# Optimization experiments

Measured on AMD Instinct MI355X. Metric: run time of the kernel, lower is better.

The kernel has to match this reference:

```python
import jax, jax.numpy as jnp
import numpy as np

N = 50000          # nodes
E_RAND = 800000    # random edges (self-loops appended -> total 850000)
F_IN = 256         # features_num
H = 128            # hidden
HEADS = 4          # headslayers
C = 40             # num_class
OUTDIM = H + HEADS * H + H  # 768, cat of [x_lin, conv1, conv2]
LRELU = 0.01       # F.leaky_relu default slope
ATT_SLOPE = 0.2    # PyG GATConv negative_slope
BN_EPS = 1e-5


def setup_inputs() -> dict:
    key = jax.random.key(0)
    ks = jax.random.split(key, 20)
    src = jax.random.randint(ks[0], (E_RAND,), 0, N)
    dst = jax.random.randint(ks[1], (E_RAND,), 0, N)
    loops = jnp.arange(N, dtype=src.dtype)
    edge_index = jnp.stack([jnp.concatenate([src, loops]),
                            jnp.concatenate([dst, loops])], axis=0)
    g = lambda k, shape, fan: jax.random.normal(k, shape, jnp.float32) * (1.0 / np.sqrt(fan))
    return {
        "x": jax.random.normal(ks[2], (N, F_IN), jnp.float32),
        "edge_index": edge_index,
        # first_lin
        "fw_W": g(ks[3], (F_IN, H), F_IN), "fw_b": jnp.zeros((H,), jnp.float32),
        # conv1: GATConv(H, H, heads=HEADS)
        "c1_W": g(ks[4], (H, HEADS * H), H),
        "c1_as": g(ks[5], (HEADS, H), H), "c1_ad": g(ks[6], (HEADS, H), H),
        "c1_b": jnp.zeros((HEADS * H,), jnp.float32),
        # conv2: GATConv(HEADS*H, H, heads=1)
        "c2_W": g(ks[7], (HEADS * H, H), HEADS * H),
        "c2_as": g(ks[8], (1, H), H), "c2_ad": g(ks[9], (1, H), H),
        "c2_b": jnp.zeros((H,), jnp.float32),
        # batchnorms (training-mode batch stats)
        "bn1_g": jnp.ones((H,), jnp.float32), "bn1_b": jnp.zeros((H,), jnp.float32),
        "bn2_g": jnp.ones((HEADS * H,), jnp.float32), "bn2_b": jnp.zeros((HEADS * H,), jnp.float32),
        "bn3_g": jnp.ones((H,), jnp.float32), "bn3_b": jnp.zeros((H,), jnp.float32),
        # lin2
        "l2_W": g(ks[10], (OUTDIM, C), OUTDIM), "l2_b": jnp.zeros((C,), jnp.float32),
    }


def _batchnorm(x, gamma, beta):
    mu = jnp.mean(x, axis=0)
    var = jnp.mean(jnp.square(x - mu), axis=0)  # biased, as torch BN training
    return (x - mu) * (gamma / jnp.sqrt(var + BN_EPS)) + beta


def _gat_conv(x, edge_index, W, a_src, a_dst, bias, heads, out_dim):
    src, dst = edge_index[0], edge_index[1]
    h = (x @ W).reshape(-1, heads, out_dim)            # [N, heads, out]
    alpha_s = jnp.sum(h * a_src, axis=-1)              # [N, heads]
    alpha_d = jnp.sum(h * a_dst, axis=-1)              # [N, heads]
    e = alpha_s[src] + alpha_d[dst]                    # [E, heads]
    e = jnp.where(e >= 0, e, ATT_SLOPE * e)            # leaky_relu(0.2)
    # segment softmax over incoming edges of each dst node
    emax = jax.ops.segment_max(e, dst, num_segments=N)
    e = jnp.exp(e - emax[dst])
    denom = jax.ops.segment_sum(e, dst, num_segments=N)
    alpha = e / (denom[dst] + 1e-16)                   # [E, heads]
    msg = h[src] * alpha[:, :, None]                   # [E, heads, out]
    out = jax.ops.segment_sum(msg, dst, num_segments=N)
    return out.reshape(-1, heads * out_dim) + bias


def _lrelu(x):
    return jnp.where(x >= 0, x, LRELU * x)


def reference(x, edge_index, fw_W, fw_b, c1_W, c1_as, c1_ad, c1_b,
              c2_W, c2_as, c2_ad, c2_b, bn1_g, bn1_b, bn2_g, bn2_b,
              bn3_g, bn3_b, l2_W, l2_b):
    h = _lrelu(x @ fw_W + fw_b)
    h = _batchnorm(h, bn1_g, bn1_b)
    feats = [h]
    h = _lrelu(_gat_conv(h, edge_index, c1_W, c1_as, c1_ad, c1_b, HEADS, H))
    h = _batchnorm(h, bn2_g, bn2_b)
    feats.append(h)
    h = _lrelu(_gat_conv(h, edge_index, c2_W, c2_as, c2_ad, c2_b, 1, H))
    h = _batchnorm(h, bn3_g, bn3_b)
    feats.append(h)
    z = jnp.concatenate(feats, axis=1) @ l2_W + l2_b
    return jax.nn.log_softmax(z, axis=-1)
```

## Files before the change

### kernel.cpp

```cpp
#include <hip/hip_runtime.h>

#define INF_F __builtin_inff()

typedef unsigned short u16;
typedef __attribute__((ext_vector_type(8))) short s16x8;
typedef __attribute__((ext_vector_type(4))) float f32x4;

union U8 { uint4 q; s16x8 v; };

__device__ __forceinline__ float b2f(u16 u) {
    union { unsigned int i; float f; } v; v.i = ((unsigned int)u) << 16; return v.f;
}
__device__ __forceinline__ u16 f2b(float f) {
    union { float f; unsigned int i; } v; v.f = f;
    unsigned int r = (v.i + 0x7FFFu + ((v.i >> 16) & 1u)) >> 16;
    return (u16)r;
}
__device__ __forceinline__ void bf2x(unsigned int p, float& lo, float& hi) {
    union { unsigned int i; float f; } a, b;
    a.i = p << 16; b.i = p & 0xFFFF0000u;
    lo = a.f; hi = b.f;
}
__device__ __forceinline__ unsigned int packbf(float lo, float hi) {
    return (unsigned int)f2b(lo) | ((unsigned int)f2b(hi) << 16);
}

__device__ __forceinline__ void pack_one(const float* __restrict__ W, int K, int N,
                                         int Npad, u16* __restrict__ pb, int idx)
{
    int k = idx / Npad, n = idx - k * Npad;
    float v = (n < N) ? W[(size_t)k * N + n] : 0.f;
    int K5 = K >> 5;
    size_t o = ((size_t)(n >> 4) * K5 + (k >> 5)) * 512
             + ((size_t)((k >> 3) & 3)) * 128 + (n & 15) * 8 + (k & 7);
    pb[o] = f2b(v);
}

__launch_bounds__(256)
__global__ void k_prep(const float* __restrict__ fw_W, const float* __restrict__ c1_W,
                       const float* __restrict__ c2_W, const float* __restrict__ l2_W,
                       u16* __restrict__ pb_l1, u16* __restrict__ pb_c1,
                       u16* __restrict__ pb_c2, u16* __restrict__ pb_f,
                       const int* __restrict__ dst, int E, int* __restrict__ counts)
{
    int idx = blockIdx.x * 256 + threadIdx.x;
    if (idx < 32768) { pack_one(fw_W, 256, 128, 128, pb_l1, idx); return; }
    idx -= 32768;
    if (idx < 65536) { pack_one(c1_W, 128, 512, 512, pb_c1, idx); return; }
    idx -= 65536;
    if (idx < 65536) { pack_one(c2_W, 512, 128, 128, pb_c2, idx); return; }
    idx -= 65536;
    if (idx < 49152) { pack_one(l2_W, 768, 40, 64, pb_f, idx); return; }
    idx -= 49152;
    if (idx < E) atomicAdd(&counts[dst[idx]], 1);
}

template<int NFRAG, bool A_FP32, bool BN_A, bool BIAS, bool LRELU, int HEADS_PB>
__launch_bounds__(256)
__global__ void k_mgemm(const void* __restrict__ Av, int lda, int K,
                        const u16* __restrict__ pb,
                        u16* __restrict__ C, int ldc, int M,
                        const float* __restrict__ scale, const float* __restrict__ shift,
                        const float* __restrict__ bias,
                        const float* __restrict__ aw_s, const float* __restrict__ aw_d,
                        float* __restrict__ as_o, float* __restrict__ ad_o, int nheads)
{
    const int tid = threadIdx.x;
    const int w = tid >> 6, l = tid & 63;
    const int lo = l & 15, hi = l >> 4;
    const int row0 = blockIdx.y * 128 + w * 32;
    if (row0 >= M) return;
    const int cb0 = blockIdx.x * NFRAG;
    const int K5 = K >> 5;

    f32x4 acc[NFRAG][2];
    #pragma unroll
    for (int i = 0; i < NFRAG; ++i)
        #pragma unroll
        for (int s = 0; s < 2; ++s) acc[i][s] = (f32x4){0.f, 0.f, 0.f, 0.f};

    int arow[2];
    #pragma unroll
    for (int s = 0; s < 2; ++s) {
        int r = row0 + s * 16 + lo;
        arow[s] = r < M ? r : M - 1;
    }

    for (int k5 = 0; k5 < K5; ++k5) {
        const int ak = k5 * 32 + hi * 8;
        s16x8 af[2];
        #pragma unroll
        for (int s = 0; s < 2; ++s) {
            float x[8];
            if (A_FP32) {
                const float* A = (const float*)Av + (size_t)arow[s] * lda + ak;
                float4 v0 = *reinterpret_cast<const float4*>(A);
                float4 v1 = *reinterpret_cast<const float4*>(A + 4);
                x[0]=v0.x; x[1]=v0.y; x[2]=v0.z; x[3]=v0.w;
                x[4]=v1.x; x[5]=v1.y; x[6]=v1.z; x[7]=v1.w;
            } else {
                uint4 q = *reinterpret_cast<const uint4*>((const u16*)Av + (size_t)arow[s] * lda + ak);
                bf2x(q.x, x[0], x[1]); bf2x(q.y, x[2], x[3]);
                bf2x(q.z, x[4], x[5]); bf2x(q.w, x[6], x[7]);
            }
            if (BN_A) {
                #pragma unroll
                for (int j = 0; j < 8; ++j) x[j] = fmaf(x[j], scale[ak + j], shift[ak + j]);
            }
            U8 au;
            au.q.x = packbf(x[0], x[1]); au.q.y = packbf(x[2], x[3]);
            au.q.z = packbf(x[4], x[5]); au.q.w = packbf(x[6], x[7]);
            af[s] = au.v;
        }
        #pragma unroll
        for (int cb = 0; cb < NFRAG; ++cb) {
            s16x8 bf = *reinterpret_cast<const s16x8*>(
                pb + ((size_t)(cb0 + cb) * K5 + k5) * 512 + l * 8);
            acc[cb][0] = __builtin_amdgcn_mfma_f32_16x16x32_bf16(af[0], bf, acc[cb][0], 0, 0, 0);
            acc[cb][1] = __builtin_amdgcn_mfma_f32_16x16x32_bf16(af[1], bf, acc[cb][1], 0, 0, 0);
        }
    }

    #pragma unroll
    for (int cb = 0; cb < NFRAG; ++cb) {
        int col = (cb0 + cb) * 16 + lo;
        #pragma unroll
        for (int s = 0; s < 2; ++s) {
            #pragma unroll
            for (int p = 0; p < 4; ++p) {
                int r = row0 + s * 16 + hi * 4 + p;
                if (r < M) {
                    float v = acc[cb][s][p];
                    if (BIAS)  v += bias[col];
                    if (LRELU) v = v >= 0.f ? v : 0.01f * v;
                    C[(size_t)r * ldc + col] = f2b(v);
                }
            }
        }
    }

    if (HEADS_PB > 0) {
        const int h = (cb0 >> 3);
        #pragma unroll
        for (int s = 0; s < 2; ++s) {
            float ps[4] = {0.f,0.f,0.f,0.f}, pd[4] = {0.f,0.f,0.f,0.f};
            #pragma unroll
            for (int cb = 0; cb < NFRAG; ++cb) {
                int col = (cb0 + cb) * 16 + lo;
                float ws = aw_s[col], wd = aw_d[col];
                #pragma unroll
                for (int p = 0; p < 4; ++p) {
                    ps[p] = fmaf(acc[cb][s][p], ws, ps[p]);
                    pd[p] = fmaf(acc[cb][s][p], wd, pd[p]);
                }
            }
            #pragma unroll
            for (int m = 1; m < 16; m <<= 1) {
                #pragma unroll
                for (int p = 0; p < 4; ++p) {
                    ps[p] += __shfl_xor(ps[p], m, 64);
                    pd[p] += __shfl_xor(pd[p], m, 64);
                }
            }
            if (lo == 0) {
                #pragma unroll
                for (int p = 0; p < 4; ++p) {
                    int r = row0 + s * 16 + hi * 4 + p;
                    if (r < M) {
                        as_o[(size_t)r * nheads + h] = ps[p];
                        ad_o[(size_t)r * nheads + h] = pd[p];
                    }
                }
            }
        }
    }
}

__launch_bounds__(256)
__global__ void k_mfinal(const u16* __restrict__ h1, const u16* __restrict__ h2,
                         const u16* __restrict__ h3,
                         const float* __restrict__ scale, const float* __restrict__ shift,
                         const u16* __restrict__ pb, const float* __restrict__ bias,
                         float* __restrict__ out, int M)
{
    const int tid = threadIdx.x;
    const int w = tid >> 6, l = tid & 63;
    const int lo = l & 15, hi = l >> 4;
    const int row0 = blockIdx.x * 128 + w * 32;
    if (row0 >= M) return;
    const int K5 = 24;

    f32x4 acc[4][2];
    #pragma unroll
    for (int i = 0; i < 4; ++i)
        #pragma unroll
        for (int s = 0; s < 2; ++s) acc[i][s] = (f32x4){0.f, 0.f, 0.f, 0.f};

    int arow[2];
    #pragma unroll
    for (int s = 0; s < 2; ++s) {
        int r = row0 + s * 16 + lo;
        arow[s] = r < M ? r : M - 1;
    }

    for (int k5 = 0; k5 < K5; ++k5) {
        const int kk = k5 * 32 + hi * 8;
        const u16* src; int ld, offk;
        if (kk < 128)      { src = h1; ld = 128; offk = kk; }
        else if (kk < 640) { src = h2; ld = 512; offk = kk - 128; }
        else               { src = h3; ld = 128; offk = kk - 640; }
        s16x8 af[2];
        #pragma unroll
        for (int s = 0; s < 2; ++s) {
            uint4 q = *reinterpret_cast<const uint4*>(src + (size_t)arow[s] * ld + offk);
            float x[8];
            bf2x(q.x, x[0], x[1]); bf2x(q.y, x[2], x[3]);
            bf2x(q.z, x[4], x[5]); bf2x(q.w, x[6], x[7]);
            #pragma unroll
            for (int j = 0; j < 8; ++j) x[j] = fmaf(x[j], scale[kk + j], shift[kk + j]);
            U8 au;
            au.q.x = packbf(x[0], x[1]); au.q.y = packbf(x[2], x[3]);
            au.q.z = packbf(x[4], x[5]); au.q.w = packbf(x[6], x[7]);
            af[s] = au.v;
        }
        #pragma unroll
        for (int cb = 0; cb < 4; ++cb) {
            s16x8 bf = *reinterpret_cast<const s16x8*>(pb + ((size_t)cb * K5 + k5) * 512 + l * 8);
            acc[cb][0] = __builtin_amdgcn_mfma_f32_16x16x32_bf16(af[0], bf, acc[cb][0], 0, 0, 0);
            acc[cb][1] = __builtin_amdgcn_mfma_f32_16x16x32_bf16(af[1], bf, acc[cb][1], 0, 0, 0);
        }
    }

    #pragma unroll
    for (int s = 0; s < 2; ++s) {
        #pragma unroll
        for (int p = 0; p < 4; ++p) {
            int r = row0 + s * 16 + hi * 4 + p;
            float z0 = acc[0][s][p] + bias[lo];
            float z1 = acc[1][s][p] + bias[16 + lo];
            float z2 = -INF_F;
            if (lo < 8) z2 = acc[2][s][p] + bias[32 + lo];
            float mx = fmaxf(fmaxf(z0, z1), z2);
            #pragma unroll
            for (int m = 1; m < 16; m <<= 1) mx = fmaxf(mx, __shfl_xor(mx, m, 64));
            float se = __expf(z0 - mx) + __expf(z1 - mx) + ((lo < 8) ? __expf(z2 - mx) : 0.f);
            #pragma unroll
            for (int m = 1; m < 16; m <<= 1) se += __shfl_xor(se, m, 64);
            float lse = mx + __logf(se);
            if (r < M) {
                out[(size_t)r * 40 + lo]      = z0 - lse;
                out[(size_t)r * 40 + 16 + lo] = z1 - lse;
                if (lo < 8) out[(size_t)r * 40 + 32 + lo] = z2 - lse;
            }
        }
    }
}

__launch_bounds__(256)
__global__ void k_colstats(const u16* __restrict__ X, int M, int C,
                           float* __restrict__ psum, float* __restrict__ psq)
{
    const int CG  = C >> 3;
    const int RPI = 256 / CG;
    const int tid = threadIdx.x;
    const int cg  = tid & (CG - 1);
    const int ro  = tid / CG;
    const int nb  = gridDim.x;
    const int rows_chunk = (M + nb - 1) / nb;
    const int r0 = blockIdx.x * rows_chunk;
    const int r1 = min(M, r0 + rows_chunk);

    float s[8] = {}, q[8] = {};
    for (int r = r0 + ro; r < r1; r += RPI) {
        uint4 u = *reinterpret_cast<const uint4*>(X + (size_t)r * C + cg * 8);
        float x[8];
        bf2x(u.x, x[0], x[1]); bf2x(u.y, x[2], x[3]);
        bf2x(u.z, x[4], x[5]); bf2x(u.w, x[6], x[7]);
        #pragma unroll
        for (int j = 0; j < 8; ++j) { s[j] += x[j]; q[j] = fmaf(x[j], x[j], q[j]); }
    }

    __shared__ float lsum[8][256];
    __shared__ float lsq [8][256];
    #pragma unroll
    for (int j = 0; j < 8; ++j) { lsum[j][tid] = s[j]; lsq[j][tid] = q[j]; }
    __syncthreads();

    if (tid < CG) {
        #pragma unroll
        for (int j = 0; j < 8; ++j) {
            float ss = 0.f, qq = 0.f;
            for (int o = 0; o < RPI; ++o) {
                ss += lsum[j][o * CG + tid];
                qq += lsq [j][o * CG + tid];
            }
            psum[(size_t)blockIdx.x * C + tid * 8 + j] = ss;
            psq [(size_t)blockIdx.x * C + tid * 8 + j] = qq;
        }
    }
}

__launch_bounds__(256)
__global__ void k_colred(const float* __restrict__ psum, const float* __restrict__ psq,
                         const float* __restrict__ g, const float* __restrict__ b,
                         int nb, int M, int C,
                         float* __restrict__ scale, float* __restrict__ shift)
{
    int c = blockIdx.x * 4 + (threadIdx.x >> 6);
    int lane = threadIdx.x & 63;
    if (c >= C) return;
    float s = 0.f, q = 0.f;
    for (int l = lane; l < nb; l += 64) {
        s += psum[(size_t)l * C + c];
        q += psq [(size_t)l * C + c];
    }
    #pragma unroll
    for (int off = 32; off; off >>= 1) {
        s += __shfl_xor(s, off, 64);
        q += __shfl_xor(q, off, 64);
    }
    if (lane == 0) {
        float mu  = s / (float)M;
        float var = q / (float)M - mu * mu;
        float sc  = g[c] * rsqrtf(var + 1e-5f);
        scale[c] = sc;
        shift[c] = b[c] - mu * sc;
    }
}

__launch_bounds__(256)
__global__ void k_scan1(const int* __restrict__ counts, int n,
                        int* __restrict__ rowstart, int* __restrict__ tilesum)
{
    const int tid = threadIdx.x;
    const int lane = tid & 63, w = tid >> 6;
    const int i0 = blockIdx.x * 1024 + tid * 4;
    int v0 = 0, v1 = 0, v2 = 0, v3 = 0;
    if (i0 + 3 < n) {
        int4 q = *reinterpret_cast<const int4*>(counts + i0);
        v0 = q.x; v1 = q.y; v2 = q.z; v3 = q.w;
    } else if (i0 < n) {
        v0 = counts[i0];
        if (i0 + 1 < n) v1 = counts[i0 + 1];
        if (i0 + 2 < n) v2 = counts[i0 + 2];
    }
    int s1 = v0 + v1, s2 = s1 + v2, s3 = s2 + v3;
    int x = s3;
    #pragma unroll
    for (int off = 1; off < 64; off <<= 1) {
        int t = __shfl_up(x, off, 64);
        if (lane >= off) x += t;
    }
    __shared__ int wsum[4];
    if (lane == 63) wsum[w] = x;
    __syncthreads();
    int woff = 0;
    #pragma unroll
    for (int i = 0; i < 4; ++i)
        if (i < w) woff += wsum[i];
    int excl = woff + x - s3;
    if (i0 + 0 < n) rowstart[i0 + 1] = excl + v0;
    if (i0 + 1 < n) rowstart[i0 + 2] = excl + s1;
    if (i0 + 2 < n) rowstart[i0 + 3] = excl + s2;
    if (i0 + 3 < n) rowstart[i0 + 4] = excl + s3;
    if (tid == 255) tilesum[blockIdx.x] = wsum[0] + wsum[1] + wsum[2] + wsum[3];
}

__launch_bounds__(256)
__global__ void k_scan3(int* __restrict__ rowstart, const int* __restrict__ tilesum, int n)
{
    const int tile = (int)((blockIdx.x * 256) >> 10);
    __shared__ int s_off;
    if (threadIdx.x < 64) {
        int lane = threadIdx.x;
        int v = (lane < tile) ? tilesum[lane] : 0;
        #pragma unroll
        for (int m = 1; m < 64; m <<= 1) v += __shfl_xor(v, m, 64);
        if (lane == 0) s_off = v;
    }
    __syncthreads();
    int i = blockIdx.x * 256 + threadIdx.x;
    if (i < n) rowstart[i + 1] += s_off;
    if (blockIdx.x == 0 && threadIdx.x == 0) rowstart[0] = 0;
}

__launch_bounds__(256)
__global__ void k_scatter(const int* __restrict__ ei, int E,
                          const int* __restrict__ rowstart,
                          int* __restrict__ fill, int* __restrict__ csr)
{
    int e = blockIdx.x * 256 + threadIdx.x;
    if (e >= E) return;
    int s = ei[e], d = ei[E + e];
    int pos = rowstart[d] + atomicAdd(&fill[d], 1);
    csr[pos] = s;
}

__launch_bounds__(256)
__global__ void k_gat_agg_h4(const u16* __restrict__ hp,
                             const float* __restrict__ as_, const float* __restrict__ ad_,
                             const int* __restrict__ rowstart, const int* __restrict__ csr,
                             const float* __restrict__ bias, u16* __restrict__ out, int Nn)
{
    int d = (int)((blockIdx.x * (size_t)blockDim.x + threadIdx.x) >> 6);
    int lane = threadIdx.x & 63;
    if (d >= Nn) return;
    const int h = lane >> 4;
    const int li = lane & 15;
    const int dim = li * 8;
    int e0 = rowstart[d], e1 = rowstart[d + 1];
    float adv = ad_[(size_t)d * 4 + h];

    float mx = -INF_F;
    for (int j = e0 + li; j < e1; j += 16) {
        int s = csr[j];
        float e = as_[(size_t)s * 4 + h] + adv;
        e = e >= 0.f ? e : 0.2f * e;
        mx = fmaxf(mx, e);
    }
    #pragma unroll
    for (int m = 1; m < 16; m <<= 1) mx = fmaxf(mx, __shfl_xor(mx, m, 64));

    float lsum = 0.f;
    float acc[8] = {};

    #define F4(J, A, U) { int jj = min((J), e1 - 1); int s_ = csr[jj];                \
        A = as_[(size_t)s_ * 4 + h];                                                  \
        U = *reinterpret_cast<const uint4*>(hp + ((size_t)s_ * 4 + h) * 128 + dim); }
    #define C4(A, U) { float e_ = A + adv; e_ = e_ >= 0.f ? e_ : 0.2f * e_;           \
        float w_ = __expf(e_ - mx); lsum += w_;                                       \
        float x_[8];                                                                  \
        bf2x(U.x, x_[0], x_[1]); bf2x(U.y, x_[2], x_[3]);                             \
        bf2x(U.z, x_[4], x_[5]); bf2x(U.w, x_[6], x_[7]);                             \
        _Pragma("unroll")                                                             \
        for (int t_ = 0; t_ < 8; ++t_) acc[t_] = fmaf(x_[t_], w_, acc[t_]); }

    float a0, a1, a2, a3, a4, a5, a6, a7;
    uint4 u0, u1, u2, u3, u4, u5, u6, u7;
    F4(e0 + 0, a0, u0); F4(e0 + 1, a1, u1); F4(e0 + 2, a2, u2); F4(e0 + 3, a3, u3);
    F4(e0 + 4, a4, u4); F4(e0 + 5, a5, u5); F4(e0 + 6, a6, u6); F4(e0 + 7, a7, u7);

    int j = e0;
    for (; j + 3 < e1; j += 4) {
        C4(a0, u0); C4(a1, u1); C4(a2, u2); C4(a3, u3);
        a0 = a4; u0 = u4; a1 = a5; u1 = u5; a2 = a6; u2 = u6; a3 = a7; u3 = u7;
        F4(j + 8, a4, u4); F4(j + 9, a5, u5); F4(j + 10, a6, u6); F4(j + 11, a7, u7);
    }
    if (j < e1)     C4(a0, u0);
    if (j + 1 < e1) C4(a1, u1);
    if (j + 2 < e1) C4(a2, u2);
    #undef F4
    #undef C4

    float inv = 1.f / (lsum + 1e-16f);
    const int ob = h * 128 + dim;
    float v[8];
    #pragma unroll
    for (int t = 0; t < 8; ++t) {
        float z = acc[t] * inv + bias[ob + t];
        v[t] = z >= 0.f ? z : 0.01f * z;
    }
    uint4 o;
    o.x = packbf(v[0], v[1]); o.y = packbf(v[2], v[3]);
    o.z = packbf(v[4], v[5]); o.w = packbf(v[6], v[7]);
    *reinterpret_cast<uint4*>(out + (size_t)d * 512 + ob) = o;
}

__launch_bounds__(256)
__global__ void k_gat_agg_h1(const u16* __restrict__ hp,
                             const float* __restrict__ as_, const float* __restrict__ ad_,
                             const int* __restrict__ rowstart, const int* __restrict__ csr,
                             const float* __restrict__ bias, u16* __restrict__ out, int Nn)
{
    int d = (int)((blockIdx.x * (size_t)blockDim.x + threadIdx.x) >> 6);
    int lane = threadIdx.x & 63;
    if (d >= Nn) return;
    const int dim = lane * 2;
    int e0 = rowstart[d], e1 = rowstart[d + 1];
    float adv = ad_[d];

    float mx = -INF_F;
    for (int j = e0 + lane; j < e1; j += 64) {
        int s = csr[j];
        float e = as_[s] + adv;
        e = e >= 0.f ? e : 0.2f * e;
        mx = fmaxf(mx, e);
    }
    #pragma unroll
    for (int m = 1; m < 64; m <<= 1) mx = fmaxf(mx, __shfl_xor(mx, m, 64));

    float lsum = 0.f, acc0 = 0.f, acc1 = 0.f;

    #define F1(J, A, U) { int jj = min((J), e1 - 1); int s_ = csr[jj];                \
        A = as_[s_];                                                                  \
        U = *reinterpret_cast<const unsigned int*>(hp + (size_t)s_ * 128 + dim); }
    #define C1(A, U) { float e_ = A + adv; e_ = e_ >= 0.f ? e_ : 0.2f * e_;           \
        float w_ = __expf(e_ - mx); float x0_, x1_; bf2x(U, x0_, x1_);                \
        lsum += w_; acc0 = fmaf(x0_, w_, acc0); acc1 = fmaf(x1_, w_, acc1); }

    float a0, a1, a2, a3, a4, a5, a6, a7;
    unsigned int u0, u1, u2, u3, u4, u5, u6, u7;
    F1(e0 + 0, a0, u0); F1(e0 + 1, a1, u1); F1(e0 + 2, a2, u2); F1(e0 + 3, a3, u3);
    F1(e0 + 4, a4, u4); F1(e0 + 5, a5, u5); F1(e0 + 6, a6, u6); F1(e0 + 7, a7, u7);

    int j = e0;
    for (; j + 3 < e1; j += 4) {
        C1(a0, u0); C1(a1, u1); C1(a2, u2); C1(a3, u3);
        a0 = a4; u0 = u4; a1 = a5; u1 = u5; a2 = a6; u2 = u6; a3 = a7; u3 = u7;
        F1(j + 8, a4, u4); F1(j + 9, a5, u5); F1(j + 10, a6, u6); F1(j + 11, a7, u7);
    }
    if (j < e1)     C1(a0, u0);
    if (j + 1 < e1) C1(a1, u1);
    if (j + 2 < e1) C1(a2, u2);
    #undef F1
    #undef C1

    float inv = 1.f / (lsum + 1e-16f);
    float v0 = acc0 * inv + bias[dim];
    float v1 = acc1 * inv + bias[dim + 1];
    v0 = v0 >= 0.f ? v0 : 0.01f * v0;
    v1 = v1 >= 0.f ? v1 : 0.01f * v1;
    *reinterpret_cast<unsigned int*>(out + (size_t)d * 128 + dim) = packbf(v0, v1);
}

extern "C" void kernel_launch(void* const* d_in, const int* in_sizes, int n_in,
                              void* d_out, int out_size, void* d_ws, size_t ws_size,
                              hipStream_t stream)
{
    const float* x     = (const float*)d_in[0];
    const int*   ei    = (const int*)  d_in[1];
    const float* fw_W  = (const float*)d_in[2];
    const float* fw_b  = (const float*)d_in[3];
    const float* c1_W  = (const float*)d_in[4];
    const float* c1_as = (const float*)d_in[5];
    const float* c1_ad = (const float*)d_in[6];
    const float* c1_b  = (const float*)d_in[7];
    const float* c2_W  = (const float*)d_in[8];
    const float* c2_as = (const float*)d_in[9];
    const float* c2_ad = (const float*)d_in[10];
    const float* c2_b  = (const float*)d_in[11];
    const float* bn1_g = (const float*)d_in[12];
    const float* bn1_b = (const float*)d_in[13];
    const float* bn2_g = (const float*)d_in[14];
    const float* bn2_b = (const float*)d_in[15];
    const float* bn3_g = (const float*)d_in[16];
    const float* bn3_b = (const float*)d_in[17];
    const float* l2_W  = (const float*)d_in[18];
    const float* l2_b  = (const float*)d_in[19];
    float* out = (float*)d_out;

    const int N = in_sizes[0] / 256;
    const int E = in_sizes[1] / 2;
    const int NB = 256;

    char* base = (char*)d_ws;
    size_t off = 0;
    auto alloc = [&](size_t bytes) -> void* {
        void* p = (void*)(base + off);
        off = (off + bytes + 255) & ~(size_t)255;
        return p;
    };
    int*   counts = (int*)  alloc((size_t)N * 4);
    int*   fill   = (int*)  alloc((size_t)N * 4);
    size_t zero_bytes = off;
    const int SCB = (N + 1023) / 1024;
    float* as1      = (float*)alloc((size_t)N * 4 * 4);
    float* ad1      = (float*)alloc((size_t)N * 4 * 4);
    float* as2      = (float*)alloc((size_t)N * 4);
    float* ad2      = (float*)alloc((size_t)N * 4);
    float* psum     = (float*)alloc((size_t)NB * 512 * 4);
    float* psq      = (float*)alloc((size_t)NB * 512 * 4);
    int*   rowstart = (int*)  alloc((size_t)(N + 1) * 4);
    int*   tilesum  = (int*)  alloc((size_t)SCB * 4);
    int*   csr      = (int*)  alloc((size_t)E * 4);
    float* scale768 = (float*)alloc(768 * 4);
    float* shift768 = (float*)alloc(768 * 4);
    u16*   pb_l1    = (u16*)  alloc((size_t)256 * 128 * 2);
    u16*   pb_c1    = (u16*)  alloc((size_t)128 * 512 * 2);
    u16*   pb_c2    = (u16*)  alloc((size_t)512 * 128 * 2);
    u16*   pb_f     = (u16*)  alloc((size_t)768 * 64 * 2);
    u16*   h1       = (u16*)  alloc((size_t)N * 128 * 2);
    u16*   h2       = (u16*)  alloc((size_t)N * 512 * 2);
    u16*   hp1      = (u16*)  alloc((size_t)N * 512 * 2);
    u16*   hp2      = hp1;
    u16*   h3       = hp1 + (size_t)N * 128;
    (void)ws_size; (void)n_in; (void)out_size;

    const int mb2 = (N + 127) / 128;
    const int wave_blocks = (int)(((size_t)N * 64 + 255) / 256);
    const int PK = 32768 + 65536 + 65536 + 49152;

    hipMemsetAsync(base, 0, zero_bytes, stream);

    k_prep<<<(PK + E + 255) / 256, 256, 0, stream>>>(
        fw_W, c1_W, c2_W, l2_W, pb_l1, pb_c1, pb_c2, pb_f, ei + E, E, counts);

    k_scan1<<<SCB, 256, 0, stream>>>(counts, N, rowstart, tilesum);
    k_scan3<<<(N + 255) / 256, 256, 0, stream>>>(rowstart, tilesum, N);

    k_scatter<<<(E + 255) / 256, 256, 0, stream>>>(ei, E, rowstart, fill, csr);

    k_mgemm<8, true, false, true, true, 0><<<dim3(1, mb2), 256, 0, stream>>>(
        x, 256, 256, pb_l1, h1, 128, N, nullptr, nullptr, fw_b,
        nullptr, nullptr, nullptr, nullptr, 0);

    k_colstats<<<NB, 256, 0, stream>>>(h1, N, 128, psum, psq);
    k_colred<<<(128 + 3) / 4, 256, 0, stream>>>(psum, psq, bn1_g, bn1_b, NB, N, 128,
                                                scale768, shift768);

    k_mgemm<8, false, true, false, false, 1><<<dim3(4, mb2), 256, 0, stream>>>(
        h1, 128, 128, pb_c1, hp1, 512, N, scale768, shift768, nullptr,
        c1_as, c1_ad, as1, ad1, 4);
    k_gat_agg_h4<<<wave_blocks, 256, 0, stream>>>(
        hp1, as1, ad1, rowstart, csr, c1_b, h2, N);

    k_colstats<<<NB, 256, 0, stream>>>(h2, N, 512, psum, psq);
    k_colred<<<(512 + 3) / 4, 256, 0, stream>>>(psum, psq, bn2_g, bn2_b, NB, N, 512,
                                                scale768 + 128, shift768 + 128);

    k_mgemm<8, false, true, false, false, 1><<<dim3(1, mb2), 256, 0, stream>>>(
        h2, 512, 512, pb_c2, hp2, 128, N, scale768 + 128, shift768 + 128, nullptr,
        c2_as, c2_ad, as2, ad2, 1);
    k_gat_agg_h1<<<wave_blocks, 256, 0, stream>>>(
        hp2, as2, ad2, rowstart, csr, c2_b, h3, N);

    k_colstats<<<NB, 256, 0, stream>>>(h3, N, 128, psum, psq);
    k_colred<<<(128 + 3) / 4, 256, 0, stream>>>(psum, psq, bn3_g, bn3_b, NB, N, 128,
                                                scale768 + 640, shift768 + 640);

    k_mfinal<<<mb2, 256, 0, stream>>>(h1, h2, h3, scale768, shift768, pb_f, l2_b, out, N);
}
```

Baseline: 453.6 us.

## Fuse CSR scatter into first GEMM launch and pack two nodes per wave in head-1 aggregation

The CSR scatter is merged into the first linear-layer GEMM as extra blocks of a single launch, so both run concurrently and one launch is removed. Zeroing of the fill counters moves from the memset into the scan kernel. The single-head GAT aggregation now handles two destination nodes per wave, 32 lanes each, with 4 features per lane and 8-byte loads, which halves wave count and widens the gathers. In exchange, the two half-waves loop to the longer of their two edge lists and mask the extra iterations.

```diff
diff --git a/kernel.cpp b/kernel.cpp
--- a/kernel.cpp
+++ b/kernel.cpp
@@ -55,13 +55,86 @@
     if (idx < E) atomicAdd(&counts[dst[idx]], 1);
 }
 
-template<int NFRAG, bool A_FP32, bool BN_A, bool BIAS, bool LRELU, int HEADS_PB>
-__launch_bounds__(256)
-__global__ void k_mgemm(const void* __restrict__ Av, int lda, int K,
+__launch_bounds__(256)
+__global__ void k_l1sc(const float* __restrict__ x, const u16* __restrict__ pb,
+                       u16* __restrict__ h1, int M, const float* __restrict__ bias,
+                       int mb2, const int* __restrict__ ei, int E,
+                       const int* __restrict__ rowstart, int* __restrict__ fill,
+                       int* __restrict__ csr)
+{
+    if ((int)blockIdx.x >= mb2) {
+        int e = ((int)blockIdx.x - mb2) * 256 + threadIdx.x;
+        if (e < E) {
+            int s = ei[e], d = ei[E + e];
+            int pos = rowstart[d] + atomicAdd(&fill[d], 1);
+            csr[pos] = s;
+        }
+        return;
+    }
+    const int tid = threadIdx.x;
+    const int w = tid >> 6, l = tid & 63;
+    const int lo = l & 15, hi = l >> 4;
+    const int row0 = blockIdx.x * 128 + w * 32;
+    if (row0 >= M) return;
+
+    f32x4 acc[8][2];
+    #pragma unroll
+    for (int i = 0; i < 8; ++i)
+        #pragma unroll
+        for (int s = 0; s < 2; ++s) acc[i][s] = (f32x4){0.f, 0.f, 0.f, 0.f};
+
+    int arow[2];
+    #pragma unroll
+    for (int s = 0; s < 2; ++s) {
+        int r = row0 + s * 16 + lo;
+        arow[s] = r < M ? r : M - 1;
+    }
+
+    for (int k5 = 0; k5 < 8; ++k5) {
+        const int ak = k5 * 32 + hi * 8;
+        s16x8 af[2];
+        #pragma unroll
+        for (int s = 0; s < 2; ++s) {
+            const float* A = x + (size_t)arow[s] * 256 + ak;
+            float4 v0 = *reinterpret_cast<const float4*>(A);
+            float4 v1 = *reinterpret_cast<const float4*>(A + 4);
+            U8 au;
+            au.q.x = packbf(v0.x, v0.y); au.q.y = packbf(v0.z, v0.w);
+            au.q.z = packbf(v1.x, v1.y); au.q.w = packbf(v1.z, v1.w);
+            af[s] = au.v;
+        }
+        #pragma unroll
+        for (int cb = 0; cb < 8; ++cb) {
+            s16x8 bf = *reinterpret_cast<const s16x8*>(pb + ((size_t)cb * 8 + k5) * 512 + l * 8);
+            acc[cb][0] = __builtin_amdgcn_mfma_f32_16x16x32_bf16(af[0], bf, acc[cb][0], 0, 0, 0);
+            acc[cb][1] = __builtin_amdgcn_mfma_f32_16x16x32_bf16(af[1], bf, acc[cb][1], 0, 0, 0);
+        }
+    }
+
+    #pragma unroll
+    for (int cb = 0; cb < 8; ++cb) {
+        int col = cb * 16 + lo;
+        #pragma unroll
+        for (int s = 0; s < 2; ++s) {
+            #pragma unroll
+            for (int p = 0; p < 4; ++p) {
+                int r = row0 + s * 16 + hi * 4 + p;
+                if (r < M) {
+                    float v = acc[cb][s][p] + bias[col];
+                    v = v >= 0.f ? v : 0.01f * v;
+                    h1[(size_t)r * 128 + col] = f2b(v);
+                }
+            }
+        }
+    }
+}
+
+template<int NFRAG, bool BN_A, int HEADS_PB>
+__launch_bounds__(256)
+__global__ void k_mgemm(const u16* __restrict__ Av, int lda, int K,
                         const u16* __restrict__ pb,
                         u16* __restrict__ C, int ldc, int M,
                         const float* __restrict__ scale, const float* __restrict__ shift,
-                        const float* __restrict__ bias,
                         const float* __restrict__ aw_s, const float* __restrict__ aw_d,
                         float* __restrict__ as_o, float* __restrict__ ad_o, int nheads)
 {
@@ -91,18 +164,10 @@
         s16x8 af[2];
         #pragma unroll
         for (int s = 0; s < 2; ++s) {
+            uint4 q = *reinterpret_cast<const uint4*>(Av + (size_t)arow[s] * lda + ak);
             float x[8];
-            if (A_FP32) {
-                const float* A = (const float*)Av + (size_t)arow[s] * lda + ak;
-                float4 v0 = *reinterpret_cast<const float4*>(A);
-                float4 v1 = *reinterpret_cast<const float4*>(A + 4);
-                x[0]=v0.x; x[1]=v0.y; x[2]=v0.z; x[3]=v0.w;
-                x[4]=v1.x; x[5]=v1.y; x[6]=v1.z; x[7]=v1.w;
-            } else {
-                uint4 q = *reinterpret_cast<const uint4*>((const u16*)Av + (size_t)arow[s] * lda + ak);
-                bf2x(q.x, x[0], x[1]); bf2x(q.y, x[2], x[3]);
-                bf2x(q.z, x[4], x[5]); bf2x(q.w, x[6], x[7]);
-            }
+            bf2x(q.x, x[0], x[1]); bf2x(q.y, x[2], x[3]);
+            bf2x(q.z, x[4], x[5]); bf2x(q.w, x[6], x[7]);
             if (BN_A) {
                 #pragma unroll
                 for (int j = 0; j < 8; ++j) x[j] = fmaf(x[j], scale[ak + j], shift[ak + j]);
@@ -129,12 +194,7 @@
             #pragma unroll
             for (int p = 0; p < 4; ++p) {
                 int r = row0 + s * 16 + hi * 4 + p;
-                if (r < M) {
-                    float v = acc[cb][s][p];
-                    if (BIAS)  v += bias[col];
-                    if (LRELU) v = v >= 0.f ? v : 0.01f * v;
-                    C[(size_t)r * ldc + col] = f2b(v);
-                }
+                if (r < M) C[(size_t)r * ldc + col] = f2b(acc[cb][s][p]);
             }
         }
     }
@@ -330,7 +390,8 @@
 
 __launch_bounds__(256)
 __global__ void k_scan1(const int* __restrict__ counts, int n,
-                        int* __restrict__ rowstart, int* __restrict__ tilesum)
+                        int* __restrict__ rowstart, int* __restrict__ tilesum,
+                        int* __restrict__ fill)
 {
     const int tid = threadIdx.x;
     const int lane = tid & 63, w = tid >> 6;
@@ -344,6 +405,15 @@
         if (i0 + 1 < n) v1 = counts[i0 + 1];
         if (i0 + 2 < n) v2 = counts[i0 + 2];
     }
+    if (i0 < n) {
+        int4 z = make_int4(0, 0, 0, 0);
+        if (i0 + 3 < n) *reinterpret_cast<int4*>(fill + i0) = z;
+        else {
+            fill[i0] = 0;
+            if (i0 + 1 < n) fill[i0 + 1] = 0;
+            if (i0 + 2 < n) fill[i0 + 2] = 0;
+        }
+    }
     int s1 = v0 + v1, s2 = s1 + v2, s3 = s2 + v3;
     int x = s3;
     #pragma unroll
@@ -382,18 +452,6 @@
     int i = blockIdx.x * 256 + threadIdx.x;
     if (i < n) rowstart[i + 1] += s_off;
     if (blockIdx.x == 0 && threadIdx.x == 0) rowstart[0] = 0;
-}
-
-__launch_bounds__(256)
-__global__ void k_scatter(const int* __restrict__ ei, int E,
-                          const int* __restrict__ rowstart,
-                          int* __restrict__ fill, int* __restrict__ csr)
-{
-    int e = blockIdx.x * 256 + threadIdx.x;
-    if (e >= E) return;
-    int s = ei[e], d = ei[E + e];
-    int pos = rowstart[d] + atomicAdd(&fill[d], 1);
-    csr[pos] = s;
 }
 
 __launch_bounds__(256)
@@ -472,55 +530,76 @@
                              const int* __restrict__ rowstart, const int* __restrict__ csr,
                              const float* __restrict__ bias, u16* __restrict__ out, int Nn)
 {
-    int d = (int)((blockIdx.x * (size_t)blockDim.x + threadIdx.x) >> 6);
-    int lane = threadIdx.x & 63;
-    if (d >= Nn) return;
-    const int dim = lane * 2;
-    int e0 = rowstart[d], e1 = rowstart[d + 1];
-    float adv = ad_[d];
+    const int lane = threadIdx.x & 63;
+    const int half = lane >> 5;
+    const int sl = lane & 31;
+    const int wave = (int)((blockIdx.x * (size_t)blockDim.x + threadIdx.x) >> 6);
+    const int d = wave * 2 + half;
+    if (wave * 2 >= Nn) return;
+    const bool act = d < Nn;
+    const int dc = act ? d : (Nn - 1);
+    const int dim = sl * 4;
+    int e0 = rowstart[dc], e1 = rowstart[dc + 1];
+    int len = e1 - e0;
+    float adv = ad_[dc];
 
     float mx = -INF_F;
-    for (int j = e0 + lane; j < e1; j += 64) {
+    for (int j = e0 + sl; j < e1; j += 32) {
         int s = csr[j];
         float e = as_[s] + adv;
         e = e >= 0.f ? e : 0.2f * e;
         mx = fmaxf(mx, e);
     }
     #pragma unroll
-    for (int m = 1; m < 64; m <<= 1) mx = fmaxf(mx, __shfl_xor(mx, m, 64));
-
-    float lsum = 0.f, acc0 = 0.f, acc1 = 0.f;
-
-    #define F1(J, A, U) { int jj = min((J), e1 - 1); int s_ = csr[jj];                \
+    for (int m = 1; m < 32; m <<= 1) mx = fmaxf(mx, __shfl_xor(mx, m, 32));
+
+    int maxlen = max(len, __shfl_xor(len, 32, 64));
+
+    float lsum = 0.f;
+    float acc[4] = {};
+
+    #define F1(JR, A, U) { int jj = e0 + min((JR), len - 1); int s_ = csr[jj];        \
         A = as_[s_];                                                                  \
-        U = *reinterpret_cast<const unsigned int*>(hp + (size_t)s_ * 128 + dim); }
-    #define C1(A, U) { float e_ = A + adv; e_ = e_ >= 0.f ? e_ : 0.2f * e_;           \
-        float w_ = __expf(e_ - mx); float x0_, x1_; bf2x(U, x0_, x1_);                \
-        lsum += w_; acc0 = fmaf(x0_, w_, acc0); acc1 = fmaf(x1_, w_, acc1); }
+        U = *reinterpret_cast<const uint2*>(hp + (size_t)s_ * 128 + dim); }
+    #define C1(JR, A, U) { float e_ = A + adv; e_ = e_ >= 0.f ? e_ : 0.2f * e_;       \
+        float w_ = ((JR) < len) ? __expf(e_ - mx) : 0.f;                              \
+        float x0_, x1_, x2_, x3_; bf2x(U.x, x0_, x1_); bf2x(U.y, x2_, x3_);           \
+        lsum += w_;                                                                   \
+        acc[0] = fmaf(x0_, w_, acc[0]); acc[1] = fmaf(x1_, w_, acc[1]);               \
+        acc[2] = fmaf(x2_, w_, acc[2]); acc[3] = fmaf(x3_, w_, acc[3]); }
 
     float a0, a1, a2, a3, a4, a5, a6, a7;
-    unsigned int u0, u1, u2, u3, u4, u5, u6, u7;
-    F1(e0 + 0, a0, u0); F1(e0 + 1, a1, u1); F1(e0 + 2, a2, u2); F1(e0 + 3, a3, u3);
-    F1(e0 + 4, a4, u4); F1(e0 + 5, a5, u5); F1(e0 + 6, a6, u6); F1(e0 + 7, a7, u7);
-
-    int j = e0;
-    for (; j + 3 < e1; j += 4) {
-        C1(a0, u0); C1(a1, u1); C1(a2, u2); C1(a3, u3);
+    uint2 u0, u1, u2, u3, u4, u5, u6, u7;
+    F1(0, a0, u0); F1(1, a1, u1); F1(2, a2, u2); F1(3, a3, u3);
+    F1(4, a4, u4); F1(5, a5, u5); F1(6, a6, u6); F1(7, a7, u7);
+
+    int jr = 0;
+    for (; jr + 3 < maxlen; jr += 4) {
+        C1(jr + 0, a0, u0); C1(jr + 1, a1, u1); C1(jr + 2, a2, u2); C1(jr + 3, a3, u3);
         a0 = a4; u0 = u4; a1 = a5; u1 = u5; a2 = a6; u2 = u6; a3 = a7; u3 = u7;
-        F1(j + 8, a4, u4); F1(j + 9, a5, u5); F1(j + 10, a6, u6); F1(j + 11, a7, u7);
-    }
-    if (j < e1)     C1(a0, u0);
-    if (j + 1 < e1) C1(a1, u1);
-    if (j + 2 < e1) C1(a2, u2);
+        F1(jr + 8, a4, u4); F1(jr + 9, a5, u5); F1(jr + 10, a6, u6); F1(jr + 11, a7, u7);
+    }
+    if (jr < maxlen)     C1(jr + 0, a0, u0);
+    if (jr + 1 < maxlen) C1(jr + 1, a1, u1);
+    if (jr + 2 < maxlen) C1(jr + 2, a2, u2);
     #undef F1
     #undef C1
 
     float inv = 1.f / (lsum + 1e-16f);
-    float v0 = acc0 * inv + bias[dim];
-    float v1 = acc1 * inv + bias[dim + 1];
+    float v0 = acc[0] * inv + bias[dim];
+    float v1 = acc[1] * inv + bias[dim + 1];
+    float v2 = acc[2] * inv + bias[dim + 2];
+    float v3 = acc[3] * inv + bias[dim + 3];
     v0 = v0 >= 0.f ? v0 : 0.01f * v0;
     v1 = v1 >= 0.f ? v1 : 0.01f * v1;
-    *reinterpret_cast<unsigned int*>(out + (size_t)d * 128 + dim) = packbf(v0, v1);
+    v2 = v2 >= 0.f ? v2 : 0.01f * v2;
+    v3 = v3 >= 0.f ? v3 : 0.01f * v3;
+    if (act) {
+        uint2 o;
+        o.x = packbf(v0, v1);
+        o.y = packbf(v2, v3);
+        *reinterpret_cast<uint2*>(out + (size_t)d * 128 + dim) = o;
+    }
 }
 
 extern "C" void kernel_launch(void* const* d_in, const int* in_sizes, int n_in,
@@ -561,9 +640,9 @@
         return p;
     };
     int*   counts = (int*)  alloc((size_t)N * 4);
-    int*   fill   = (int*)  alloc((size_t)N * 4);
     size_t zero_bytes = off;
     const int SCB = (N + 1023) / 1024;
+    int*   fill     = (int*)  alloc((size_t)N * 4);
     float* as1      = (float*)alloc((size_t)N * 4 * 4);
     float* ad1      = (float*)alloc((size_t)N * 4 * 4);
     float* as2      = (float*)alloc((size_t)N * 4);
@@ -587,7 +666,9 @@
     (void)ws_size; (void)n_in; (void)out_size;
 
     const int mb2 = (N + 127) / 128;
+    const int scb = (E + 255) / 256;
     const int wave_blocks = (int)(((size_t)N * 64 + 255) / 256);
+    const int h1_wave_blocks = (int)((((size_t)N + 1) / 2 * 64 + 255) / 256);
     const int PK = 32768 + 65536 + 65536 + 49152;
 
     hipMemsetAsync(base, 0, zero_bytes, stream);
@@ -595,21 +676,18 @@
     k_prep<<<(PK + E + 255) / 256, 256, 0, stream>>>(
         fw_W, c1_W, c2_W, l2_W, pb_l1, pb_c1, pb_c2, pb_f, ei + E, E, counts);
 
-    k_scan1<<<SCB, 256, 0, stream>>>(counts, N, rowstart, tilesum);
+    k_scan1<<<SCB, 256, 0, stream>>>(counts, N, rowstart, tilesum, fill);
     k_scan3<<<(N + 255) / 256, 256, 0, stream>>>(rowstart, tilesum, N);
 
-    k_scatter<<<(E + 255) / 256, 256, 0, stream>>>(ei, E, rowstart, fill, csr);
-
-    k_mgemm<8, true, false, true, true, 0><<<dim3(1, mb2), 256, 0, stream>>>(
-        x, 256, 256, pb_l1, h1, 128, N, nullptr, nullptr, fw_b,
-        nullptr, nullptr, nullptr, nullptr, 0);
+    k_l1sc<<<mb2 + scb, 256, 0, stream>>>(
+        x, pb_l1, h1, N, fw_b, mb2, ei, E, rowstart, fill, csr);
 
     k_colstats<<<NB, 256, 0, stream>>>(h1, N, 128, psum, psq);
     k_colred<<<(128 + 3) / 4, 256, 0, stream>>>(psum, psq, bn1_g, bn1_b, NB, N, 128,
                                                 scale768, shift768);
 
-    k_mgemm<8, false, true, false, false, 1><<<dim3(4, mb2), 256, 0, stream>>>(
-        h1, 128, 128, pb_c1, hp1, 512, N, scale768, shift768, nullptr,
+    k_mgemm<8, true, 1><<<dim3(4, mb2), 256, 0, stream>>>(
+        h1, 128, 128, pb_c1, hp1, 512, N, scale768, shift768,
         c1_as, c1_ad, as1, ad1, 4);
     k_gat_agg_h4<<<wave_blocks, 256, 0, stream>>>(
         hp1, as1, ad1, rowstart, csr, c1_b, h2, N);
@@ -618,10 +696,10 @@
     k_colred<<<(512 + 3) / 4, 256, 0, stream>>>(psum, psq, bn2_g, bn2_b, NB, N, 512,
                                                 scale768 + 128, shift768 + 128);
 
-    k_mgemm<8, false, true, false, false, 1><<<dim3(1, mb2), 256, 0, stream>>>(
-        h2, 512, 512, pb_c2, hp2, 128, N, scale768 + 128, shift768 + 128, nullptr,
+    k_mgemm<8, true, 1><<<dim3(1, mb2), 256, 0, stream>>>(
+        h2, 512, 512, pb_c2, hp2, 128, N, scale768 + 128, shift768 + 128,
         c2_as, c2_ad, as2, ad2, 1);
-    k_gat_agg_h1<<<wave_blocks, 256, 0, stream>>>(
+    k_gat_agg_h1<<<h1_wave_blocks, 256, 0, stream>>>(
         hp2, as2, ad2, rowstart, csr, c2_b, h3, N);
 
     k_colstats<<<NB, 256, 0, stream>>>(h3, N, 128, psum, psq);
```

Result: faster. 412.0 us (median of 2 runs) (-9.2%).
